# Performance work log

Measured on AMD Instinct MI355X. Metric: run time of the kernel, lower is better.

The kernel has to match this reference:

```python
import jax, jax.numpy as jnp
import numpy as np

N_NODES = 50000
N_EDGES = 800000
D_IN = 128
D_H = 128
N_LAYERS = 3
N_CLASSES = 10
NUM_GRAPHS = 256
BN_EPS = 1e-5


def _bn(h, gamma, beta):
    # BatchNorm1d, training-mode statistics (biased variance) over node axis
    mu = jnp.mean(h, axis=0)
    var = jnp.mean((h - mu) ** 2, axis=0)
    return (h - mu) * jax.lax.rsqrt(var + BN_EPS) * gamma + beta


def setup_inputs() -> dict:
    key = jax.random.key(0)
    ks = jax.random.split(key, 16)
    x = jax.random.normal(ks[0], (N_NODES, D_IN), dtype=jnp.float32)
    edge_index = jax.random.randint(ks[1], (2, N_EDGES), 0, N_NODES, dtype=jnp.int64)
    batch = jnp.sort(jax.random.randint(ks[2], (N_NODES,), 0, NUM_GRAPHS, dtype=jnp.int64))
    s1 = 1.0 / np.sqrt(D_IN)
    s2 = 1.0 / np.sqrt(D_H)
    W1 = jax.random.uniform(ks[3], (N_LAYERS, D_IN, D_H), jnp.float32, -s1, s1)
    b1 = jax.random.uniform(ks[4], (N_LAYERS, D_H), jnp.float32, -s1, s1)
    g1 = jnp.ones((N_LAYERS, D_H), jnp.float32)
    bt1 = jnp.zeros((N_LAYERS, D_H), jnp.float32)
    W2 = jax.random.uniform(ks[5], (N_LAYERS, D_H, D_H), jnp.float32, -s2, s2)
    b2 = jax.random.uniform(ks[6], (N_LAYERS, D_H), jnp.float32, -s2, s2)
    g2 = jnp.ones((N_LAYERS, D_H), jnp.float32)
    bt2 = jnp.zeros((N_LAYERS, D_H), jnp.float32)
    sc = 1.0 / np.sqrt(D_H * N_LAYERS)
    Wc1 = jax.random.uniform(ks[7], (D_H * N_LAYERS, D_H), jnp.float32, -sc, sc)
    bc1 = jax.random.uniform(ks[8], (D_H,), jnp.float32, -sc, sc)
    Wc2 = jax.random.uniform(ks[9], (D_H, N_CLASSES), jnp.float32, -s2, s2)
    bc2 = jax.random.uniform(ks[10], (N_CLASSES,), jnp.float32, -s2, s2)
    return {"x": x, "edge_index": edge_index, "batch": batch,
            "W1": W1, "b1": b1, "g1": g1, "bt1": bt1,
            "W2": W2, "b2": b2, "g2": g2, "bt2": bt2,
            "Wc1": Wc1, "bc1": bc1, "Wc2": Wc2, "bc2": bc2}


def reference(x, edge_index, batch, W1, b1, g1, bt1, W2, b2, g2, bt2, Wc1, bc1, Wc2, bc2):
    src = edge_index[0]
    dst = edge_index[1]
    readouts = []
    h = x
    for i in range(N_LAYERS):
        # GINConv, eps=0: (1+eps)*h + sum_{j->i} h_j, then MLP
        agg = jax.ops.segment_sum(h[src], dst, num_segments=N_NODES)  # [N, d]
        z = h + agg
        z = z @ W1[i] + b1[i]
        z = jax.nn.relu(_bn(z, g1[i], bt1[i]))
        z = z @ W2[i] + b2[i]
        # outer BN + ReLU
        h = jax.nn.relu(_bn(z, g2[i], bt2[i]))
        readouts.append(jax.ops.segment_sum(h, batch, num_segments=NUM_GRAPHS))
    h_graph = jnp.concatenate(readouts, axis=1)  # [G, L*d]
    # classifier (dropout in eval mode -> identity)
    out = jax.nn.relu(h_graph @ Wc1 + bc1) @ Wc2 + bc2
    return out
```

## Files before the change

kernel.cpp:

```cpp
#include <hip/hip_runtime.h>

#define N_NODES 50000
#define N_EDGES 800000
#define D 128
#define NLAYERS 3
#define N_CLASSES 10
#define NUM_GRAPHS 256
#define BN_EPS 1e-5f

#define CHUNKS 64
#define CHSIZE 12500
#define RANGES 4
#define RSIZE 12500
#define SBANKS 8
#define NBLK 196
#define SLICE 800000

typedef __attribute__((ext_vector_type(4))) float f4;
typedef __attribute__((ext_vector_type(2))) float f2;
typedef __attribute__((ext_vector_type(4))) int i4;
typedef __attribute__((ext_vector_type(8))) short short8;
typedef __attribute__((ext_vector_type(4))) unsigned short us4;
typedef __attribute__((ext_vector_type(8))) unsigned short us8;

__device__ inline float b2f(unsigned short u) {
    unsigned int i = ((unsigned int)u) << 16;
    return __builtin_bit_cast(float, i);
}
__device__ inline unsigned short f2b(float f) {
    unsigned int u = __builtin_bit_cast(unsigned int, f);
    unsigned int r = (u + 0x7FFFu + ((u >> 16) & 1u)) >> 16;
    return (unsigned short)r;
}


__device__ inline void coef_to_lds(const float* __restrict__ stats,
                                   const float* __restrict__ g,
                                   const float* __restrict__ bt,
                                   float* ac_sm, int tid) {
    if (tid < D) {
        float s = 0.f, q = 0.f;
#pragma unroll
        for (int b = 0; b < SBANKS; b++) {
            s += stats[b * 2 * D + tid];
            q += stats[b * 2 * D + D + tid];
        }
        float mu = s * (1.0f / N_NODES);
        float var = q * (1.0f / N_NODES) - mu * mu;
        float inv = rsqrtf(var + BN_EPS);
        float a = g[tid] * inv;
        ac_sm[tid] = a;
        ac_sm[D + tid] = bt[tid] - mu * a;
    }
}


__global__ __launch_bounds__(256) void k_ph(const int* __restrict__ dst,
                                            unsigned short* __restrict__ pos,
                                            int* __restrict__ ph) {
    __shared__ int h[RSIZE];
    int c = blockIdx.x, r = blockIdx.y;
    int t = threadIdx.x;
    for (int i = t; i < RSIZE; i += 256) h[i] = 0;
    __syncthreads();
    int base = c * CHSIZE;
    int lo = r * RSIZE;
    const i4* dst4 = (const i4*)(dst + base);
    for (int j = t; j < CHSIZE / 4; j += 256) {
        i4 dv = dst4[j];
#pragma unroll
        for (int u = 0; u < 4; u++) {
            int d = dv[u] - lo;
            if ((unsigned)d < RSIZE) pos[base + j * 4 + u] = (unsigned short)atomicAdd(&h[d], 1);
        }
    }
    __syncthreads();
    int* outp = ph + (size_t)c * N_NODES + lo;
    for (int i = t; i < RSIZE; i += 256) outp[i] = h[i];
}

__global__ __launch_bounds__(256) void k_m1(int* __restrict__ ph,
                                            const int* __restrict__ bat,
                                            int* __restrict__ deg,
                                            int* __restrict__ bsum,
                                            int* __restrict__ gp,
                                            int* __restrict__ bh) {
    __shared__ int sm[256];
    __shared__ int hist[64];
    int t = threadIdx.x;
    if (t < 64) hist[t] = 0;
    int b = blockIdx.x * 256 + t;
    int s = 0;
    if (b < N_NODES) {
#pragma unroll 4
        for (int c = 0; c < CHUNKS; c++) {
            int v = ph[(size_t)c * N_NODES + b];
            ph[(size_t)c * N_NODES + b] = s;
            s += v;
        }
        deg[b] = s;
    }
    sm[t] = s;
    __syncthreads();
    if (b < N_NODES) atomicAdd(&hist[min(s, 63)], 1);
    for (int off = 128; off > 0; off >>= 1) {
        if (t < off) sm[t] += sm[t + off];
        __syncthreads();
    }
    if (t == 0) bsum[blockIdx.x] = sm[0];
    if (t < 64) bh[blockIdx.x * 64 + t] = hist[t];
    if (b < N_NODES) {
        int bb = bat[b];
        int prev = (b == 0) ? -1 : bat[b - 1];
        for (int g = prev + 1; g <= bb; g++) gp[g] = b;
        if (b == N_NODES - 1)
            for (int g = bb + 1; g <= NUM_GRAPHS; g++) gp[g] = N_NODES;
    }
}


__global__ __launch_bounds__(256) void k_xw(const float* __restrict__ x,
                                            const float* __restrict__ W1,
                                            const float* __restrict__ W2,
                                            unsigned short* __restrict__ xb,
                                            short8* __restrict__ Wb) {
    int gid = blockIdx.x * 256 + threadIdx.x;
    const f4* xf = (const f4*)x;
#pragma unroll
    for (int rep = 0; rep < 2; rep++) {
        int i = gid + rep * 800000;
        f4 v = xf[i];
        us4 o;
        o[0] = f2b(v.x); o[1] = f2b(v.y); o[2] = f2b(v.z); o[3] = f2b(v.w);
        int n = i >> 5;
        int f0 = (i & 31) * 4;
        *(us4*)(xb + (size_t)(f0 >> 4) * SLICE + (size_t)n * 16 + (f0 & 15)) = o;
    }
    if (gid < 6 * 32 * 64) {
        int m = gid >> 11;
        int f = (gid >> 6) & 31;
        int l = gid & 63;
        int ct = f >> 2, ks = f & 3;
        int n = ct * 16 + (l & 15);
        int k0 = ks * 32 + (l >> 4) * 8;
        const float* Wsrc = (m < 3) ? (W1 + (size_t)m * D * D) : (W2 + (size_t)(m - 3) * D * D);
        short8 o;
#pragma unroll
        for (int j = 0; j < 8; j++) o[j] = (short)f2b(Wsrc[(size_t)(k0 + j) * D + n]);
        Wb[gid] = o;
    }
}


__global__ void k_s2(int* __restrict__ bsum, int* __restrict__ rowp, int* __restrict__ bh) {
    __shared__ int sm[256];
    int t = threadIdx.x;
    int v = (t < NBLK) ? bsum[t] : 0;
    sm[t] = v;
    __syncthreads();
    for (int off = 1; off < 256; off <<= 1) {
        int u = (t >= off) ? sm[t - off] : 0;
        __syncthreads();
        sm[t] += u;
        __syncthreads();
    }
    if (t < NBLK) bsum[t] = sm[t] - v;
    if (t == NBLK - 1) rowp[N_NODES] = sm[t];
    __syncthreads();
    int tot = 0;
    if (t < 64) {
        for (int blk = 0; blk < NBLK; blk++) tot += bh[blk * 64 + t];
    }
    sm[t] = (t < 64) ? tot : 0;
    __syncthreads();
    for (int off = 1; off < 64; off <<= 1) {
        int u = (t >= off && t < 64) ? sm[t - off] : 0;
        __syncthreads();
        if (t < 64) sm[t] += u;
        __syncthreads();
    }
    if (t < 64) {
        int run = sm[t] - tot;
        for (int blk = 0; blk < NBLK; blk++) {
            int tmp = bh[blk * 64 + t];
            bh[blk * 64 + t] = run;
            run += tmp;
        }
    }
}


__global__ void k_s3(const int* __restrict__ deg, const int* __restrict__ bsum,
                     int* __restrict__ rowp, const int* __restrict__ bh,
                     unsigned short* __restrict__ perm) {
    __shared__ int sm[256];
    __shared__ int lh[64];
    int t = threadIdx.x;
    if (t < 64) lh[t] = 0;
    int i = blockIdx.x * 256 + t;
    int v = (i < N_NODES) ? deg[i] : 0;
    sm[t] = v;
    __syncthreads();
    for (int off = 1; off < 256; off <<= 1) {
        int u = (t >= off) ? sm[t - off] : 0;
        __syncthreads();
        sm[t] += u;
        __syncthreads();
    }
    if (i < N_NODES) {
        rowp[i] = bsum[blockIdx.x] + sm[t] - v;
        int bk = min(v, 63);
        int p = atomicAdd(&lh[bk], 1);
        perm[bh[blockIdx.x * 64 + bk] + p] = (unsigned short)i;
    }
}

__global__ __launch_bounds__(256) void k_scatter(const int* __restrict__ src,
                                                 const int* __restrict__ dst,
                                                 const unsigned short* __restrict__ pos,
                                                 const int* __restrict__ ph,
                                                 const int* __restrict__ rowp,
                                                 unsigned short* __restrict__ csr) {
    int e0 = (blockIdx.x * 256 + threadIdx.x) * 4;
    if (e0 >= N_EDGES) return;
    i4 sv = *(const i4*)(src + e0);
    i4 dv = *(const i4*)(dst + e0);
    us4 pv = *(const us4*)(pos + e0);
#pragma unroll
    for (int u = 0; u < 4; u++) {
        int cc = (e0 + u) / CHSIZE;
        int d = dv[u];
        csr[rowp[d] + ph[(size_t)cc * N_NODES + d] + (int)pv[u]] = (unsigned short)sv[u];
    }
}


template <bool APPLY_T>
__global__ __launch_bounds__(256) void k_agg(const unsigned short* __restrict__ H,
                                             const float* __restrict__ stats,
                                             const float* __restrict__ g,
                                             const float* __restrict__ bt,
                                             const int* __restrict__ rowp,
                                             const unsigned short* __restrict__ csr,
                                             const unsigned short* __restrict__ perm,
                                             unsigned short* __restrict__ U) {
    __shared__ float ac_sm[2 * D];
    int tid = threadIdx.x;
    if (APPLY_T) {
        coef_to_lds(stats, g, bt, ac_sm, tid);
        __syncthreads();
    }
    int s = blockIdx.x & 7;
    int chunk = blockIdx.x >> 3;
    int li = chunk * 128 + (tid >> 1);
    if (li >= N_NODES) return;
    int node = perm[li];
    int lane = tid & 1;
    const unsigned short* Hs = H + (size_t)s * SLICE;
    unsigned short* Us = U + (size_t)s * SLICE;
    float av[8], cv[8];
    if (APPLY_T) {
        int f0 = s * 16 + lane * 8;
#pragma unroll
        for (int i = 0; i < 8; i++) {
            av[i] = ac_sm[f0 + i];
            cv[i] = ac_sm[D + f0 + i];
        }
    }
    float acc[8] = {0.f, 0.f, 0.f, 0.f, 0.f, 0.f, 0.f, 0.f};
    auto accum = [&](us8 v) {
#pragma unroll
        for (int i = 0; i < 8; i++) {
            float f = b2f(v[i]);
            if (APPLY_T) f = fmaxf(f * av[i] + cv[i], 0.f);
            acc[i] += f;
        }
    };
    accum(*(const us8*)(Hs + (size_t)node * 16 + lane * 8));
    int beg = rowp[node], end = rowp[node + 1];
    int j = beg;
    for (; j + 8 <= end; j += 8) {
        int idx[8];
#pragma unroll
        for (int u = 0; u < 8; u++) idx[u] = csr[j + u];
        us8 v[8];
#pragma unroll
        for (int u = 0; u < 8; u++) v[u] = *(const us8*)(Hs + (size_t)idx[u] * 16 + lane * 8);
#pragma unroll
        for (int u = 0; u < 8; u++) accum(v[u]);
    }
    for (; j < end; j++) accum(*(const us8*)(Hs + (size_t)csr[j] * 16 + lane * 8));
    us8 o;
#pragma unroll
    for (int i = 0; i < 8; i++) o[i] = f2b(acc[i]);
    *(us8*)(Us + (size_t)node * 16 + lane * 8) = o;
}


template <bool TRANS>
__global__ __launch_bounds__(256) void k_gemm(const unsigned short* __restrict__ A,
                                              const short8* __restrict__ Wb,
                                              const float* __restrict__ bias,
                                              const float* __restrict__ stats_in,
                                              const float* __restrict__ g,
                                              const float* __restrict__ bt,
                                              unsigned short* __restrict__ Z,
                                              float* __restrict__ stats_out, int M) {
    __shared__ float lds_s[D], lds_q[D];
    __shared__ float ac_sm[2 * D];
    int tid = threadIdx.x;
    if (tid < D) { lds_s[tid] = 0.f; lds_q[tid] = 0.f; }
    if (TRANS) coef_to_lds(stats_in, g, bt, ac_sm, tid);
    int w = tid >> 6, l = tid & 63;
    int lr = l & 15, lg = l >> 4;
    int rowb0 = blockIdx.x * 128 + w * 32;
    f4 acc[2][8];
#pragma unroll
    for (int ct = 0; ct < 8; ct++) {
        float bv = bias[ct * 16 + lr];
#pragma unroll
        for (int rt = 0; rt < 2; rt++) {
            acc[rt][ct].x = bv; acc[rt][ct].y = bv; acc[rt][ct].z = bv; acc[rt][ct].w = bv;
        }
    }
    __syncthreads();

#pragma unroll
    for (int ks = 0; ks < 4; ks++) {
        short8 a[2];
        int k0 = ks * 32 + lg * 8;
        const unsigned short* As = A + (size_t)(k0 >> 4) * SLICE + (k0 & 15);
#pragma unroll
        for (int rt = 0; rt < 2; rt++) {
            int arow = rowb0 + rt * 16 + lr;
            int arow_c = arow < M ? arow : M - 1;
            const unsigned short* ap = As + (size_t)arow_c * 16;
            if (!TRANS) {
                a[rt] = *(const short8*)ap;
            } else {
                us4 v0 = *(const us4*)ap;
                us4 v1 = *(const us4*)(ap + 4);
                f4 a0 = *(const f4*)&ac_sm[k0];
                f4 a1 = *(const f4*)&ac_sm[k0 + 4];
                f4 c0 = *(const f4*)&ac_sm[D + k0];
                f4 c1 = *(const f4*)&ac_sm[D + k0 + 4];
                a[rt][0] = (short)f2b(fmaxf(b2f(v0[0]) * a0.x + c0.x, 0.f));
                a[rt][1] = (short)f2b(fmaxf(b2f(v0[1]) * a0.y + c0.y, 0.f));
                a[rt][2] = (short)f2b(fmaxf(b2f(v0[2]) * a0.z + c0.z, 0.f));
                a[rt][3] = (short)f2b(fmaxf(b2f(v0[3]) * a0.w + c0.w, 0.f));
                a[rt][4] = (short)f2b(fmaxf(b2f(v1[0]) * a1.x + c1.x, 0.f));
                a[rt][5] = (short)f2b(fmaxf(b2f(v1[1]) * a1.y + c1.y, 0.f));
                a[rt][6] = (short)f2b(fmaxf(b2f(v1[2]) * a1.z + c1.z, 0.f));
                a[rt][7] = (short)f2b(fmaxf(b2f(v1[3]) * a1.w + c1.w, 0.f));
            }
        }
#pragma unroll
        for (int ct = 0; ct < 8; ct++) {
            short8 b = Wb[(ct * 4 + ks) * 64 + l];
            acc[0][ct] = __builtin_amdgcn_mfma_f32_16x16x32_bf16(a[0], b, acc[0][ct], 0, 0, 0);
            acc[1][ct] = __builtin_amdgcn_mfma_f32_16x16x32_bf16(a[1], b, acc[1][ct], 0, 0, 0);
        }
    }

#pragma unroll
    for (int ct = 0; ct < 8; ct++) {
        float s = 0.f, q = 0.f;
        unsigned short* Zs = Z + (size_t)ct * SLICE + lr;
#pragma unroll
        for (int rt = 0; rt < 2; rt++) {
#pragma unroll
            for (int r = 0; r < 4; r++) {
                float v = acc[rt][ct][r];
                int rd = rowb0 + rt * 16 + lg * 4 + r;
                float m = rd < M ? 1.f : 0.f;
                s += v * m;
                q += v * v * m;
                if (rd < M) Zs[(size_t)rd * 16] = f2b(v);
            }
        }
        s += __shfl_xor(s, 16);
        s += __shfl_xor(s, 32);
        q += __shfl_xor(q, 16);
        q += __shfl_xor(q, 32);
        if (lg == 0) {
            atomicAdd(&lds_s[ct * 16 + lr], s);
            atomicAdd(&lds_q[ct * 16 + lr], q);
        }
    }
    __syncthreads();
    int bank = blockIdx.x & (SBANKS - 1);
    if (tid < D) {
        atomicAdd(&stats_out[bank * 2 * D + tid], lds_s[tid]);
        atomicAdd(&stats_out[bank * 2 * D + D + tid], lds_q[tid]);
    }
}


__global__ __launch_bounds__(256) void k_readout(const unsigned short* __restrict__ Zb,
                                                 const float* __restrict__ stats,
                                                 const float* __restrict__ g,
                                                 const float* __restrict__ bt,
                                                 const int* __restrict__ gp,
                                                 const int* __restrict__ batch,
                                                 float* __restrict__ ro, int layer) {
    __shared__ f2 sm[256];
    __shared__ float ac_sm[2 * D];
    int tid = threadIdx.x;
    coef_to_lds(stats, g, bt, ac_sm, tid);
    __syncthreads();
    int n0 = blockIdx.x * 256;
    int n1 = n0 + 256; if (n1 > N_NODES) n1 = N_NODES;
    int g_lo = batch[n0], g_hi = batch[n1 - 1];
    int grp = tid >> 6, cw = tid & 63;
    const unsigned short* Zs = Zb + (size_t)(cw >> 3) * SLICE + ((2 * cw) & 15);
    float a0 = ac_sm[2 * cw], a1 = ac_sm[2 * cw + 1];
    float c0 = ac_sm[D + 2 * cw], c1 = ac_sm[D + 2 * cw + 1];
    for (int gg = g_lo; gg <= g_hi; gg++) {
        int beg = gp[gg]; if (beg < n0) beg = n0;
        int end = gp[gg + 1]; if (end > n1) end = n1;
        f2 acc; acc.x = 0.f; acc.y = 0.f;
        for (int r = beg + grp; r < end; r += 4) {
            unsigned int v = *(const unsigned int*)(Zs + (size_t)r * 16);
            float x0 = b2f((unsigned short)(v & 0xFFFFu));
            float x1 = b2f((unsigned short)(v >> 16));
            acc.x += fmaxf(x0 * a0 + c0, 0.f);
            acc.y += fmaxf(x1 * a1 + c1, 0.f);
        }
        sm[tid] = acc;
        __syncthreads();
        if (tid < 64) {
            f2 t = sm[tid];
            t.x += sm[tid + 64].x + sm[tid + 128].x + sm[tid + 192].x;
            t.y += sm[tid + 64].y + sm[tid + 128].y + sm[tid + 192].y;
            atomicAdd(&ro[(size_t)gg * (NLAYERS * D) + layer * D + 2 * cw], t.x);
            atomicAdd(&ro[(size_t)gg * (NLAYERS * D) + layer * D + 2 * cw + 1], t.y);
        }
        __syncthreads();
    }
}


__global__ void k_cls(const float* __restrict__ ro, const float* __restrict__ Wc1,
                      const float* __restrict__ bc1, const float* __restrict__ Wc2,
                      const float* __restrict__ bc2, float* __restrict__ out) {
    __shared__ float r_sm[NLAYERS * D];
    __shared__ float h_sm[D];
    int g = blockIdx.x;
    int t = threadIdx.x;
    for (int i = t; i < NLAYERS * D; i += D) r_sm[i] = ro[(size_t)g * (NLAYERS * D) + i];
    __syncthreads();
    float acc = bc1[t];
    for (int k = 0; k < NLAYERS * D; k++) acc += r_sm[k] * Wc1[(size_t)k * D + t];
    h_sm[t] = fmaxf(acc, 0.f);
    __syncthreads();
    if (t < N_CLASSES) {
        float o = bc2[t];
        for (int k = 0; k < D; k++) o += h_sm[k] * Wc2[k * N_CLASSES + t];
        out[g * N_CLASSES + t] = o;
    }
}


extern "C" void kernel_launch(void* const* d_in, const int* in_sizes, int n_in,
                              void* d_out, int out_size, void* d_ws, size_t ws_size,
                              hipStream_t stream) {
    const float* x   = (const float*)d_in[0];
    const int*   ei  = (const int*)d_in[1];
    const int*   bat = (const int*)d_in[2];
    const float* W1  = (const float*)d_in[3];
    const float* b1  = (const float*)d_in[4];
    const float* g1  = (const float*)d_in[5];
    const float* bt1 = (const float*)d_in[6];
    const float* W2  = (const float*)d_in[7];
    const float* b2  = (const float*)d_in[8];
    const float* g2  = (const float*)d_in[9];
    const float* bt2 = (const float*)d_in[10];
    const float* Wc1 = (const float*)d_in[11];
    const float* bc1 = (const float*)d_in[12];
    const float* Wc2 = (const float*)d_in[13];
    const float* bc2 = (const float*)d_in[14];
    float* out = (float*)d_out;

    const int* src = ei;
    const int* dst = ei + N_EDGES;

    char* ws = (char*)d_ws;
    size_t off = 0;
    auto alloc = [&](size_t bytes) -> void* {
        void* p = ws + off;
        off += (bytes + 255) & ~(size_t)255;
        return p;
    };
    float* stats = (float*)alloc(6 * SBANKS * 2 * D * sizeof(float));
    float* ro    = (float*)alloc((size_t)NUM_GRAPHS * NLAYERS * D * sizeof(float));
    size_t zero_bytes = off;
    int*   deg   = (int*)alloc(N_NODES * sizeof(int));
    int*   gp    = (int*)alloc((NUM_GRAPHS + 1) * sizeof(int));
    int*   bsum  = (int*)alloc(256 * sizeof(int));
    int*   rowp  = (int*)alloc((N_NODES + 1) * sizeof(int));
    int*   bh    = (int*)alloc(NBLK * 64 * sizeof(int));
    unsigned short* pos  = (unsigned short*)alloc(N_EDGES * sizeof(unsigned short));
    unsigned short* csr  = (unsigned short*)alloc(N_EDGES * sizeof(unsigned short));
    unsigned short* perm = (unsigned short*)alloc(N_NODES * sizeof(unsigned short));
    const size_t NBH = (size_t)N_NODES * D * sizeof(unsigned short);
    unsigned short* xb   = (unsigned short*)alloc(NBH);
    unsigned short* bufA = (unsigned short*)alloc(NBH);
    unsigned short* bufB = (unsigned short*)alloc(NBH);
    unsigned short* bufC = (unsigned short*)alloc(NBH);
    short8* Wb   = (short8*)alloc(6 * 32 * 64 * sizeof(short8));
    int* ph = (int*)bufB;

    hipMemsetAsync(ws, 0, zero_bytes, stream);

    k_ph<<<dim3(CHUNKS, RANGES), 256, 0, stream>>>(dst, pos, ph);
    k_m1<<<NBLK, 256, 0, stream>>>(ph, bat, deg, bsum, gp, bh);
    k_xw<<<3125, 256, 0, stream>>>(x, W1, W2, xb, Wb);
    k_s2<<<1, 256, 0, stream>>>(bsum, rowp, bh);
    k_s3<<<NBLK, 256, 0, stream>>>(deg, bsum, rowp, bh, perm);
    k_scatter<<<(N_EDGES / 4 + 255) / 256, 256, 0, stream>>>(src, dst, pos, ph, rowp, csr);

    const int agg_grid  = 8 * ((N_NODES + 127) / 128);
    const int gemm_grid = (N_NODES + 127) / 128;
    const unsigned short* H = xb;
    for (int i = 0; i < NLAYERS; i++) {
        float* st1 = stats + (size_t)(2 * i) * SBANKS * 2 * D;
        float* st2 = stats + (size_t)(2 * i + 1) * SBANKS * 2 * D;
        float* st2p = stats + (size_t)(2 * i - 1) * SBANKS * 2 * D;
        if (i == 0)
            k_agg<false><<<agg_grid, 256, 0, stream>>>(H, nullptr, nullptr, nullptr,
                                                       rowp, csr, perm, bufA);
        else
            k_agg<true><<<agg_grid, 256, 0, stream>>>(H, st2p, g2 + (i - 1) * D,
                                                      bt2 + (i - 1) * D, rowp, csr, perm, bufA);
        k_gemm<false><<<gemm_grid, 256, 0, stream>>>(bufA, Wb + (size_t)i * 2048, b1 + i * D,
                                                     nullptr, nullptr, nullptr, bufB, st1, N_NODES);
        k_gemm<true><<<gemm_grid, 256, 0, stream>>>(bufB, Wb + (size_t)(3 + i) * 2048, b2 + i * D,
                                                    st1, g1 + i * D, bt1 + i * D, bufC, st2, N_NODES);
        k_readout<<<NBLK, 256, 0, stream>>>(bufC, st2, g2 + i * D, bt2 + i * D,
                                            gp, bat, ro, i);
        H = bufC;
    }
    k_cls<<<NUM_GRAPHS, 128, 0, stream>>>(ro, Wc1, bc1, Wc2, bc2, out);
}
```

Baseline: 371.7 us.

## Switch node features from sliced to row-major layout with 16-lane aggregation

Replaces the 8-slice feature layout (16 features per slice, one block per slice) with a plain row-major bf16 layout, and changes aggregation so 16 lanes cooperatively gather a full 256-byte row per neighbor instead of 2 lanes per slice across 8 separate grid passes. GEMM, readout and conversion kernels are updated to index the row-major layout. The per-chunk prefix histogram is also narrowed from int to unsigned short, which shrinks that intermediate buffer's traffic. The aim is fewer redundant reads of the CSR index and row pointers and wider contiguous gathers, at the cost of less L2 locality per slice.

```diff
diff --git a/kernel.cpp b/kernel.cpp
--- a/kernel.cpp
+++ b/kernel.cpp
@@ -14,7 +14,6 @@
 #define RSIZE 12500
 #define SBANKS 8
 #define NBLK 196
-#define SLICE 800000
 
 typedef __attribute__((ext_vector_type(4))) float f4;
 typedef __attribute__((ext_vector_type(2))) float f2;
@@ -33,7 +32,6 @@
     return (unsigned short)r;
 }
 
-
 __device__ inline void coef_to_lds(const float* __restrict__ stats,
                                    const float* __restrict__ g,
                                    const float* __restrict__ bt,
@@ -57,7 +55,7 @@
 
 __global__ __launch_bounds__(256) void k_ph(const int* __restrict__ dst,
                                             unsigned short* __restrict__ pos,
-                                            int* __restrict__ ph) {
+                                            unsigned short* __restrict__ ph) {
     __shared__ int h[RSIZE];
     int c = blockIdx.x, r = blockIdx.y;
     int t = threadIdx.x;
@@ -75,11 +73,11 @@
         }
     }
     __syncthreads();
-    int* outp = ph + (size_t)c * N_NODES + lo;
-    for (int i = t; i < RSIZE; i += 256) outp[i] = h[i];
-}
-
-__global__ __launch_bounds__(256) void k_m1(int* __restrict__ ph,
+    unsigned short* outp = ph + (size_t)c * N_NODES + lo;
+    for (int i = t; i < RSIZE; i += 256) outp[i] = (unsigned short)h[i];
+}
+
+__global__ __launch_bounds__(256) void k_m1(unsigned short* __restrict__ ph,
                                             const int* __restrict__ bat,
                                             int* __restrict__ deg,
                                             int* __restrict__ bsum,
@@ -95,7 +93,7 @@
 #pragma unroll 4
         for (int c = 0; c < CHUNKS; c++) {
             int v = ph[(size_t)c * N_NODES + b];
-            ph[(size_t)c * N_NODES + b] = s;
+            ph[(size_t)c * N_NODES + b] = (unsigned short)s;
             s += v;
         }
         deg[b] = s;
@@ -122,7 +120,7 @@
 __global__ __launch_bounds__(256) void k_xw(const float* __restrict__ x,
                                             const float* __restrict__ W1,
                                             const float* __restrict__ W2,
-                                            unsigned short* __restrict__ xb,
+                                            us4* __restrict__ xb,
                                             short8* __restrict__ Wb) {
     int gid = blockIdx.x * 256 + threadIdx.x;
     const f4* xf = (const f4*)x;
@@ -132,9 +130,7 @@
         f4 v = xf[i];
         us4 o;
         o[0] = f2b(v.x); o[1] = f2b(v.y); o[2] = f2b(v.z); o[3] = f2b(v.w);
-        int n = i >> 5;
-        int f0 = (i & 31) * 4;
-        *(us4*)(xb + (size_t)(f0 >> 4) * SLICE + (size_t)n * 16 + (f0 & 15)) = o;
+        xb[i] = o;
     }
     if (gid < 6 * 32 * 64) {
         int m = gid >> 11;
@@ -218,7 +214,7 @@
 __global__ __launch_bounds__(256) void k_scatter(const int* __restrict__ src,
                                                  const int* __restrict__ dst,
                                                  const unsigned short* __restrict__ pos,
-                                                 const int* __restrict__ ph,
+                                                 const unsigned short* __restrict__ ph,
                                                  const int* __restrict__ rowp,
                                                  unsigned short* __restrict__ csr) {
     int e0 = (blockIdx.x * 256 + threadIdx.x) * 4;
@@ -230,53 +226,47 @@
     for (int u = 0; u < 4; u++) {
         int cc = (e0 + u) / CHSIZE;
         int d = dv[u];
-        csr[rowp[d] + ph[(size_t)cc * N_NODES + d] + (int)pv[u]] = (unsigned short)sv[u];
+        csr[rowp[d] + (int)ph[(size_t)cc * N_NODES + d] + (int)pv[u]] = (unsigned short)sv[u];
     }
 }
 
 
 template <bool APPLY_T>
-__global__ __launch_bounds__(256) void k_agg(const unsigned short* __restrict__ H,
+__global__ __launch_bounds__(256) void k_agg(const us8* __restrict__ H,
                                              const float* __restrict__ stats,
                                              const float* __restrict__ g,
                                              const float* __restrict__ bt,
                                              const int* __restrict__ rowp,
                                              const unsigned short* __restrict__ csr,
                                              const unsigned short* __restrict__ perm,
-                                             unsigned short* __restrict__ U) {
+                                             us8* __restrict__ U) {
     __shared__ float ac_sm[2 * D];
     int tid = threadIdx.x;
     if (APPLY_T) {
         coef_to_lds(stats, g, bt, ac_sm, tid);
         __syncthreads();
     }
-    int s = blockIdx.x & 7;
-    int chunk = blockIdx.x >> 3;
-    int li = chunk * 128 + (tid >> 1);
-    if (li >= N_NODES) return;
-    int node = perm[li];
-    int lane = tid & 1;
-    const unsigned short* Hs = H + (size_t)s * SLICE;
-    unsigned short* Us = U + (size_t)s * SLICE;
+    int gid = blockIdx.x * 256 + tid;
+    int node = perm[gid >> 4];
+    int lane = tid & 15;
     float av[8], cv[8];
     if (APPLY_T) {
-        int f0 = s * 16 + lane * 8;
 #pragma unroll
         for (int i = 0; i < 8; i++) {
-            av[i] = ac_sm[f0 + i];
-            cv[i] = ac_sm[D + f0 + i];
-        }
-    }
-    float acc[8] = {0.f, 0.f, 0.f, 0.f, 0.f, 0.f, 0.f, 0.f};
+            av[i] = ac_sm[lane * 8 + i];
+            cv[i] = ac_sm[D + lane * 8 + i];
+        }
+    }
+    float s[8] = {0.f, 0.f, 0.f, 0.f, 0.f, 0.f, 0.f, 0.f};
     auto accum = [&](us8 v) {
 #pragma unroll
         for (int i = 0; i < 8; i++) {
             float f = b2f(v[i]);
             if (APPLY_T) f = fmaxf(f * av[i] + cv[i], 0.f);
-            acc[i] += f;
+            s[i] += f;
         }
     };
-    accum(*(const us8*)(Hs + (size_t)node * 16 + lane * 8));
+    accum(H[(size_t)node * 16 + lane]);
     int beg = rowp[node], end = rowp[node + 1];
     int j = beg;
     for (; j + 8 <= end; j += 8) {
@@ -285,15 +275,21 @@
         for (int u = 0; u < 8; u++) idx[u] = csr[j + u];
         us8 v[8];
 #pragma unroll
-        for (int u = 0; u < 8; u++) v[u] = *(const us8*)(Hs + (size_t)idx[u] * 16 + lane * 8);
+        for (int u = 0; u < 8; u++) v[u] = H[(size_t)idx[u] * 16 + lane];
 #pragma unroll
         for (int u = 0; u < 8; u++) accum(v[u]);
     }
-    for (; j < end; j++) accum(*(const us8*)(Hs + (size_t)csr[j] * 16 + lane * 8));
+    for (; j + 2 <= end; j += 2) {
+        int i0 = csr[j], i1 = csr[j + 1];
+        us8 v0 = H[(size_t)i0 * 16 + lane];
+        us8 v1 = H[(size_t)i1 * 16 + lane];
+        accum(v0); accum(v1);
+    }
+    if (j < end) accum(H[(size_t)csr[j] * 16 + lane]);
     us8 o;
 #pragma unroll
-    for (int i = 0; i < 8; i++) o[i] = f2b(acc[i]);
-    *(us8*)(Us + (size_t)node * 16 + lane * 8) = o;
+    for (int i = 0; i < 8; i++) o[i] = f2b(s[i]);
+    U[(size_t)node * 16 + lane] = o;
 }
 
 
@@ -328,16 +324,15 @@
 #pragma unroll
     for (int ks = 0; ks < 4; ks++) {
         short8 a[2];
-        int k0 = ks * 32 + lg * 8;
-        const unsigned short* As = A + (size_t)(k0 >> 4) * SLICE + (k0 & 15);
 #pragma unroll
         for (int rt = 0; rt < 2; rt++) {
             int arow = rowb0 + rt * 16 + lr;
             int arow_c = arow < M ? arow : M - 1;
-            const unsigned short* ap = As + (size_t)arow_c * 16;
             if (!TRANS) {
-                a[rt] = *(const short8*)ap;
+                a[rt] = *(const short8*)(A + (size_t)arow_c * D + ks * 32 + lg * 8);
             } else {
+                int k0 = ks * 32 + lg * 8;
+                const unsigned short* ap = A + (size_t)arow_c * D + k0;
                 us4 v0 = *(const us4*)ap;
                 us4 v1 = *(const us4*)(ap + 4);
                 f4 a0 = *(const f4*)&ac_sm[k0];
@@ -365,7 +360,6 @@
 #pragma unroll
     for (int ct = 0; ct < 8; ct++) {
         float s = 0.f, q = 0.f;
-        unsigned short* Zs = Z + (size_t)ct * SLICE + lr;
 #pragma unroll
         for (int rt = 0; rt < 2; rt++) {
 #pragma unroll
@@ -375,7 +369,7 @@
                 float m = rd < M ? 1.f : 0.f;
                 s += v * m;
                 q += v * v * m;
-                if (rd < M) Zs[(size_t)rd * 16] = f2b(v);
+                if (rd < M) Z[(size_t)rd * D + ct * 16 + lr] = f2b(v);
             }
         }
         s += __shfl_xor(s, 16);
@@ -396,7 +390,7 @@
 }
 
 
-__global__ __launch_bounds__(256) void k_readout(const unsigned short* __restrict__ Zb,
+__global__ __launch_bounds__(256) void k_readout(const unsigned int* __restrict__ Zb,
                                                  const float* __restrict__ stats,
                                                  const float* __restrict__ g,
                                                  const float* __restrict__ bt,
@@ -412,7 +406,6 @@
     int n1 = n0 + 256; if (n1 > N_NODES) n1 = N_NODES;
     int g_lo = batch[n0], g_hi = batch[n1 - 1];
     int grp = tid >> 6, cw = tid & 63;
-    const unsigned short* Zs = Zb + (size_t)(cw >> 3) * SLICE + ((2 * cw) & 15);
     float a0 = ac_sm[2 * cw], a1 = ac_sm[2 * cw + 1];
     float c0 = ac_sm[D + 2 * cw], c1 = ac_sm[D + 2 * cw + 1];
     for (int gg = g_lo; gg <= g_hi; gg++) {
@@ -420,7 +413,7 @@
         int end = gp[gg + 1]; if (end > n1) end = n1;
         f2 acc; acc.x = 0.f; acc.y = 0.f;
         for (int r = beg + grp; r < end; r += 4) {
-            unsigned int v = *(const unsigned int*)(Zs + (size_t)r * 16);
+            unsigned int v = Zb[(size_t)r * 64 + cw];
             float x0 = b2f((unsigned short)(v & 0xFFFFu));
             float x1 = b2f((unsigned short)(v >> 16));
             acc.x += fmaxf(x0 * a0 + c0, 0.f);
@@ -508,18 +501,18 @@
     unsigned short* bufB = (unsigned short*)alloc(NBH);
     unsigned short* bufC = (unsigned short*)alloc(NBH);
     short8* Wb   = (short8*)alloc(6 * 32 * 64 * sizeof(short8));
-    int* ph = (int*)bufB;
+    unsigned short* ph = (unsigned short*)bufB;
 
     hipMemsetAsync(ws, 0, zero_bytes, stream);
 
     k_ph<<<dim3(CHUNKS, RANGES), 256, 0, stream>>>(dst, pos, ph);
     k_m1<<<NBLK, 256, 0, stream>>>(ph, bat, deg, bsum, gp, bh);
-    k_xw<<<3125, 256, 0, stream>>>(x, W1, W2, xb, Wb);
+    k_xw<<<3125, 256, 0, stream>>>(x, W1, W2, (us4*)xb, Wb);
     k_s2<<<1, 256, 0, stream>>>(bsum, rowp, bh);
     k_s3<<<NBLK, 256, 0, stream>>>(deg, bsum, rowp, bh, perm);
     k_scatter<<<(N_EDGES / 4 + 255) / 256, 256, 0, stream>>>(src, dst, pos, ph, rowp, csr);
 
-    const int agg_grid  = 8 * ((N_NODES + 127) / 128);
+    const int agg_grid  = N_NODES * 16 / 256;
     const int gemm_grid = (N_NODES + 127) / 128;
     const unsigned short* H = xb;
     for (int i = 0; i < NLAYERS; i++) {
@@ -527,16 +520,16 @@
         float* st2 = stats + (size_t)(2 * i + 1) * SBANKS * 2 * D;
         float* st2p = stats + (size_t)(2 * i - 1) * SBANKS * 2 * D;
         if (i == 0)
-            k_agg<false><<<agg_grid, 256, 0, stream>>>(H, nullptr, nullptr, nullptr,
-                                                       rowp, csr, perm, bufA);
+            k_agg<false><<<agg_grid, 256, 0, stream>>>((const us8*)H, nullptr, nullptr, nullptr,
+                                                       rowp, csr, perm, (us8*)bufA);
         else
-            k_agg<true><<<agg_grid, 256, 0, stream>>>(H, st2p, g2 + (i - 1) * D,
-                                                      bt2 + (i - 1) * D, rowp, csr, perm, bufA);
+            k_agg<true><<<agg_grid, 256, 0, stream>>>((const us8*)H, st2p, g2 + (i - 1) * D,
+                                                      bt2 + (i - 1) * D, rowp, csr, perm, (us8*)bufA);
         k_gemm<false><<<gemm_grid, 256, 0, stream>>>(bufA, Wb + (size_t)i * 2048, b1 + i * D,
                                                      nullptr, nullptr, nullptr, bufB, st1, N_NODES);
         k_gemm<true><<<gemm_grid, 256, 0, stream>>>(bufB, Wb + (size_t)(3 + i) * 2048, b2 + i * D,
                                                     st1, g1 + i * D, bt1 + i * D, bufC, st2, N_NODES);
-        k_readout<<<NBLK, 256, 0, stream>>>(bufC, st2, g2 + i * D, bt2 + i * D,
+        k_readout<<<NBLK, 256, 0, stream>>>((const unsigned int*)bufC, st2, g2 + i * D, bt2 + i * D,
                                             gp, bat, ro, i);
         H = bufC;
     }
```

Result: faster. 334.2 us (-10.1%).
